# Optimization experiments

Measured on AMD Instinct MI355X. Metric: run time of the kernel, lower is better.

Reference implementation:

```python
import jax, jax.numpy as jnp
import numpy as np

# Junction tree: C0=(X0,X1f,X2), C1=(X1c,X2,X3f), C2=(X2,X3c,X4)
D0, D1F, D1C, D2, D3F, D3C, D4 = 256, 1024, 256, 256, 512, 256, 512


def _sel(fine: int, coarse: int) -> jnp.ndarray:
    """0/1 selection matrix [fine, coarse]: M[f, f // (fine//coarse)] = 1.
    Equivalent to torch_to_matrix_mul(arange(fine), arange(fine)//r, fine, coarse)."""
    r = fine // coarse
    return (jnp.arange(fine)[:, None] // r == jnp.arange(coarse)[None, :]).astype(jnp.float32)


def setup_inputs() -> dict:
    key = jax.random.key(0)
    k0, k1, k2 = jax.random.split(key, 3)
    theta0 = jax.random.normal(k0, (D0, D1F, D2), dtype=jnp.float32)
    theta1 = jax.random.normal(k1, (D1C, D2, D3F), dtype=jnp.float32)
    theta2 = jax.random.normal(k2, (D2, D3C, D4), dtype=jnp.float32)
    m_x1_fwd = _sel(D1F, D1C)          # (1024, 256): fine X1 -> coarse X1
    m_x1_bwd = m_x1_fwd.T              # (256, 1024): coarse X1 -> fine X1
    m_x3_fwd = _sel(D3F, D3C)          # (512, 256)
    m_x3_bwd = m_x3_fwd.T              # (256, 512)
    return dict(theta0=theta0, theta1=theta1, theta2=theta2,
                m_x1_fwd=m_x1_fwd, m_x1_bwd=m_x1_bwd,
                m_x3_fwd=m_x3_fwd, m_x3_bwd=m_x3_bwd)


def reference(theta0, theta1, theta2, m_x1_fwd, m_x1_bwd, m_x3_fwd, m_x3_bwd):
    # --- forward message C0 -> C1: sum over X0, map X1 fine->coarse, X2 passthrough
    msg01 = jnp.einsum('jc,jf->fc', theta0.sum(axis=0), m_x1_fwd)   # (D1C, D2)
    theta1 = theta1 + msg01[:, :, None]                             # reshape_dims (T,T,F)
    # --- forward message C1 -> C2: sum over X1, X2 passthrough, map X3 fine->coarse
    msg12 = jnp.einsum('cj,jf->cf', theta1.sum(axis=0), m_x3_fwd)   # (D2, D3C)
    theta2 = theta2 + msg12[:, :, None]
    # --- backward message C2 -> C1: sum over X4, subtract stored fwd msg, map X3 coarse->fine
    msg21 = jnp.einsum('cj,jf->cf', theta2.sum(axis=2) - msg12, m_x3_bwd)  # (D2, D3F)
    theta1 = theta1 + msg21[None, :, :]                             # reshape_dims (F,T,T)
    # --- backward message C1 -> C0: sum over X3, subtract stored fwd msg, map X1 coarse->fine
    msg10 = jnp.einsum('jc,jf->fc', theta1.sum(axis=2) - msg01, m_x1_bwd)  # (D1F, D2)
    theta0 = theta0 + msg10[None, :, :]
    return (theta0, theta1, theta2)
```

## Files before the change

### kernel.cpp

```cpp
#include <hip/hip_runtime.h>

#define D0   256
#define D1F  1024
#define D1C  256
#define D2   256
#define D3F  512
#define D3C  256
#define D4   512

#define OFF_MSG01 0
#define OFF_S10   65536
#define OFF_S12   196608
#define OFF_S22   262144
#define OFF_MSG12 327680
#define OFF_S2    393216
#define OFF_S3    458752

__global__ __launch_bounds__(256) void k_r0(const float* __restrict__ t0,
                                            float* __restrict__ ws) {
  float* msg01 = ws + OFF_MSG01;
  const int f = blockIdx.x, ic = blockIdx.y, t = threadIdx.x;
  const int c4 = t & 63, r = t >> 6;
  const float4* t0v = (const float4*)t0;
  const int j = 4 * f + r;
  float4 acc = make_float4(0.f, 0.f, 0.f, 0.f);
#pragma unroll
  for (int it = 0; it < 16; ++it) {
    const int i = ic * 16 + it;
    float4 v = t0v[((size_t)i * D1F + j) * 64 + c4];
    acc.x += v.x; acc.y += v.y; acc.z += v.z; acc.w += v.w;
  }
  __shared__ float4 lds[256];
  lds[t] = acc;
  __syncthreads();
  if (t < 64) {
    float4 a0 = lds[t], a1 = lds[t + 64], a2 = lds[t + 128], a3 = lds[t + 192];
    float* dst = &msg01[f * D2 + 4 * t];
    atomicAdd(dst + 0, a0.x + a1.x + a2.x + a3.x);
    atomicAdd(dst + 1, a0.y + a1.y + a2.y + a3.y);
    atomicAdd(dst + 2, a0.z + a1.z + a2.z + a3.z);
    atomicAdd(dst + 3, a0.w + a1.w + a2.w + a3.w);
  }
}

__global__ __launch_bounds__(256) void k_r1(const float* __restrict__ t1,
                                            float* __restrict__ ws) {
  float* S10 = ws + OFF_S10;
  float* S12 = ws + OFF_S12;
  const int c = blockIdx.x, ac = blockIdx.y, t = threadIdx.x;
  const int lane = t & 63, w = t >> 6;
  __shared__ float red[4];
  float sx = 0.f, sy = 0.f;
  for (int aa = 0; aa < 16; ++aa) {
    const int a = ac * 16 + aa;
    const float2* row = (const float2*)(t1 + ((size_t)a * D2 + c) * D3F);
    float2 v = row[t];
    sx += v.x; sy += v.y;
    float p = v.x + v.y;
#pragma unroll
    for (int off = 32; off; off >>= 1) p += __shfl_down(p, off);
    if (lane == 0) red[w] = p;
    __syncthreads();
    if (t == 0) S12[a * D2 + c] = red[0] + red[1] + red[2] + red[3];
    __syncthreads();
  }
  atomicAdd(&S10[c * D3F + 2 * t + 0], sx);
  atomicAdd(&S10[c * D3F + 2 * t + 1], sy);
}

__global__ __launch_bounds__(256) void k_msg12(float* __restrict__ ws) {
  const float* msg01 = ws + OFF_MSG01;
  const float* S10   = ws + OFF_S10;
  float* msg12       = ws + OFF_MSG12;
  const int c = blockIdx.x, t = threadIdx.x;
  float p = msg01[t * D2 + c];
#pragma unroll
  for (int off = 32; off; off >>= 1) p += __shfl_down(p, off);
  __shared__ float red[4];
  if ((t & 63) == 0) red[t >> 6] = p;
  __syncthreads();
  const float colA = red[0] + red[1] + red[2] + red[3];
  msg12[c * D3C + t] = S10[c * D3F + 2 * t] + S10[c * D3F + 2 * t + 1] + 2.f * colA;
}

__global__ __launch_bounds__(256) void k_w2(const float* __restrict__ t2,
                                            float* __restrict__ out2,
                                            float* __restrict__ ws) {
  const float* msg12 = ws + OFF_MSG12;
  float* S22         = ws + OFF_S22;
  const int c = blockIdx.x, fc = blockIdx.y, t = threadIdx.x;
  const int lane = t & 63, w = t >> 6;
  __shared__ float red[4];
  for (int ff = 0; ff < 16; ++ff) {
    const int f = fc * 16 + ff;
    const size_t base = ((size_t)c * D3C + f) * D4;
    float2 v = ((const float2*)(t2 + base))[t];
    const float m = msg12[c * D3C + f];
    float2 o; o.x = v.x + m; o.y = v.y + m;
    ((float2*)(out2 + base))[t] = o;
    float p = v.x + v.y;
#pragma unroll
    for (int off = 32; off; off >>= 1) p += __shfl_down(p, off);
    if (lane == 0) red[w] = p;
    __syncthreads();
    if (t == 0) S22[c * D3C + f] = red[0] + red[1] + red[2] + red[3];
    __syncthreads();
  }
}

__global__ __launch_bounds__(256) void k_s3(float* __restrict__ ws) {
  const float* msg01 = ws + OFF_MSG01;
  const float* S12   = ws + OFF_S12;
  const float* S22   = ws + OFF_S22;
  const float* msg12 = ws + OFF_MSG12;
  float* s2          = ws + OFF_S2;
  float* s3          = ws + OFF_S3;
  const int c = blockIdx.x, t = threadIdx.x;
  const float m12 = msg12[c * D3C + t];
  const float s2v = S22[c * D3C + t] + 511.f * m12;
  s2[c * D3C + t] = s2v;
  float p = s2v;
#pragma unroll
  for (int off = 32; off; off >>= 1) p += __shfl_down(p, off);
  __shared__ float red[4];
  if ((t & 63) == 0) red[t >> 6] = p;
  __syncthreads();
  const float rs = red[0] + red[1] + red[2] + red[3];
  s3[t * D2 + c] = S12[t * D2 + c] + 511.f * msg01[t * D2 + c] + 2.f * rs;
}

__global__ __launch_bounds__(256) void k_w1(const float* __restrict__ t1,
                                            float* __restrict__ out1,
                                            const float* __restrict__ ws) {
  const float* msg01 = ws + OFF_MSG01;
  const float* s2    = ws + OFF_S2;
  const size_t idx = (size_t)blockIdx.x * 256 + threadIdx.x;
  const int k4 = (int)(idx & 127);
  const int c  = (int)((idx >> 7) & 255);
  const int a  = (int)(idx >> 15);
  float4 v = ((const float4*)t1)[idx];
  const float m  = msg01[a * D2 + c];
  const float sa = s2[c * D3C + 2 * k4];
  const float sb = s2[c * D3C + 2 * k4 + 1];
  float4 o;
  o.x = v.x + m + sa; o.y = v.y + m + sa;
  o.z = v.z + m + sb; o.w = v.w + m + sb;
  ((float4*)out1)[idx] = o;
}

__global__ __launch_bounds__(256) void k_w0(const float* __restrict__ t0,
                                            float* __restrict__ out0,
                                            const float* __restrict__ ws) {
  const float4* s3v = (const float4*)(ws + OFF_S3);
  const size_t idx = (size_t)blockIdx.x * 256 + threadIdx.x;
  const int c4 = (int)(idx & 63);
  const int j  = (int)((idx >> 6) & 1023);
  float4 v = ((const float4*)t0)[idx];
  float4 m = s3v[(j >> 2) * 64 + c4];
  float4 o;
  o.x = v.x + m.x; o.y = v.y + m.y; o.z = v.z + m.z; o.w = v.w + m.w;
  ((float4*)out0)[idx] = o;
}

extern "C" void kernel_launch(void* const* d_in, const int* in_sizes, int n_in,
                              void* d_out, int out_size, void* d_ws, size_t ws_size,
                              hipStream_t stream) {
  const float* t0 = (const float*)d_in[0];
  const float* t1 = (const float*)d_in[1];
  const float* t2 = (const float*)d_in[2];
  float* out0 = (float*)d_out;
  float* out1 = out0 + (size_t)D0 * D1F * D2;
  float* out2 = out1 + (size_t)D1C * D2 * D3F;
  float* ws = (float*)d_ws;

  hipMemsetAsync(d_ws, 0, (size_t)OFF_S12 * sizeof(float), stream);

  k_r0<<<dim3(256, 16), 256, 0, stream>>>(t0, ws);
  k_r1<<<dim3(256, 16), 256, 0, stream>>>(t1, ws);
  k_msg12<<<256, 256, 0, stream>>>(ws);
  k_w2<<<dim3(256, 16), 256, 0, stream>>>(t2, out2, ws);
  k_s3<<<256, 256, 0, stream>>>(ws);
  k_w1<<<32768, 256, 0, stream>>>(t1, out1, ws);
  k_w0<<<65536, 256, 0, stream>>>(t0, out0, ws);
}
```

Measured before the change: 943.2 us.

## Chunk computation over X2 to reuse theta slices in cache and fuse kernels

Splits the whole pipeline into four chunks along the X2 axis so each chunk's theta0/theta1 slices are reduced and then rewritten while still likely resident in the large last-level cache. Merges the reduction kernels and message computations into fewer launches, and uses nontemporal stores for outputs to avoid polluting cache. Adds more launches and narrower per-row accesses in theta0 (64-byte segments), which may reduce coalescing efficiency.

Measured after the change: 958.0 us. Within noise of the previous version (+1.6%).

```diff
diff --git a/kernel.cpp b/kernel.cpp
--- a/kernel.cpp
+++ b/kernel.cpp
@@ -8,158 +8,180 @@
 #define D3C  256
 #define D4   512
 
+#define CB   64
+#define NCB  4
+
 #define OFF_MSG01 0
 #define OFF_S10   65536
 #define OFF_S12   196608
 #define OFF_S22   262144
 #define OFF_MSG12 327680
-#define OFF_S2    393216
-#define OFF_S3    458752
-
-__global__ __launch_bounds__(256) void k_r0(const float* __restrict__ t0,
-                                            float* __restrict__ ws) {
-  float* msg01 = ws + OFF_MSG01;
-  const int f = blockIdx.x, ic = blockIdx.y, t = threadIdx.x;
-  const int c4 = t & 63, r = t >> 6;
-  const float4* t0v = (const float4*)t0;
-  const int j = 4 * f + r;
-  float4 acc = make_float4(0.f, 0.f, 0.f, 0.f);
-#pragma unroll
-  for (int it = 0; it < 16; ++it) {
-    const int i = ic * 16 + it;
-    float4 v = t0v[((size_t)i * D1F + j) * 64 + c4];
-    acc.x += v.x; acc.y += v.y; acc.z += v.z; acc.w += v.w;
-  }
-  __shared__ float4 lds[256];
-  lds[t] = acc;
-  __syncthreads();
-  if (t < 64) {
-    float4 a0 = lds[t], a1 = lds[t + 64], a2 = lds[t + 128], a3 = lds[t + 192];
-    float* dst = &msg01[f * D2 + 4 * t];
-    atomicAdd(dst + 0, a0.x + a1.x + a2.x + a3.x);
-    atomicAdd(dst + 1, a0.y + a1.y + a2.y + a3.y);
-    atomicAdd(dst + 2, a0.z + a1.z + a2.z + a3.z);
-    atomicAdd(dst + 3, a0.w + a1.w + a2.w + a3.w);
-  }
-}
-
-__global__ __launch_bounds__(256) void k_r1(const float* __restrict__ t1,
-                                            float* __restrict__ ws) {
-  float* S10 = ws + OFF_S10;
-  float* S12 = ws + OFF_S12;
-  const int c = blockIdx.x, ac = blockIdx.y, t = threadIdx.x;
-  const int lane = t & 63, w = t >> 6;
+#define OFF_S3    393216
+
+typedef float f4 __attribute__((ext_vector_type(4)));
+
+__device__ __forceinline__ float wave_sum(float s) {
+#pragma unroll
+  for (int off = 32; off; off >>= 1) s += __shfl_down(s, off);
+  return s;
+}
+__device__ __forceinline__ float wave_allsum(float s) {
+#pragma unroll
+  for (int off = 32; off; off >>= 1) s += __shfl_xor(s, off);
+  return s;
+}
+
+__global__ __launch_bounds__(256) void k_stage1(const float* __restrict__ t0,
+                                                const float* __restrict__ t1,
+                                                float* __restrict__ ws, int cb) {
+  const int t = threadIdx.x, lane = t & 63, w = t >> 6;
+  __shared__ f4 lds[4][2][64];
+  if (blockIdx.x < 1024) {
+    const int bx = blockIdx.x;
+    const int c  = cb * CB + (bx & 63);
+    const int ac = bx >> 6;
+    float* S10 = ws + OFF_S10;
+    float* S12 = ws + OFF_S12;
+    f4 accA = {0.f, 0.f, 0.f, 0.f};
+    f4 accB = {0.f, 0.f, 0.f, 0.f};
+#pragma unroll
+    for (int ii = 0; ii < 4; ++ii) {
+      const int a = ac * 16 + ii * 4 + w;
+      const f4* row = (const f4*)(t1 + ((size_t)a * D2 + c) * D3F);
+      f4 v0 = row[lane];
+      f4 v1 = row[lane + 64];
+      accA += v0; accB += v1;
+      float s = v0.x + v0.y + v0.z + v0.w + v1.x + v1.y + v1.z + v1.w;
+      s = wave_sum(s);
+      if (lane == 0) S12[a * D2 + c] = s;
+    }
+    lds[w][0][lane] = accA;
+    lds[w][1][lane] = accB;
+    __syncthreads();
+    if (t < 128) {
+      const int which = t >> 6, l = t & 63;
+      f4 s = lds[0][which][l] + lds[1][which][l] + lds[2][which][l] + lds[3][which][l];
+      float* dst = &S10[(size_t)c * D3F + which * 256 + 4 * l];
+      atomicAdd(dst + 0, s.x);
+      atomicAdd(dst + 1, s.y);
+      atomicAdd(dst + 2, s.z);
+      atomicAdd(dst + 3, s.w);
+    }
+  } else {
+    const int bx = blockIdx.x - 1024;
+    const int f = bx & 255, ic = bx >> 8;
+    float* msg01 = ws + OFF_MSG01;
+    const int c4 = lane & 15, jr = lane >> 4;
+    const int j = 4 * f + jr;
+    const f4* t0v = (const f4*)t0;
+    f4 acc = {0.f, 0.f, 0.f, 0.f};
+#pragma unroll
+    for (int ii = 0; ii < 4; ++ii) {
+      const int i = ic * 16 + w * 4 + ii;
+      acc += t0v[((size_t)i * D1F + j) * 64 + cb * 16 + c4];
+    }
+#pragma unroll
+    for (int off = 32; off >= 16; off >>= 1) {
+      acc.x += __shfl_down(acc.x, off);
+      acc.y += __shfl_down(acc.y, off);
+      acc.z += __shfl_down(acc.z, off);
+      acc.w += __shfl_down(acc.w, off);
+    }
+    if (jr == 0) lds[w][0][c4] = acc;
+    __syncthreads();
+    if (t < 16) {
+      f4 s = lds[0][0][t] + lds[1][0][t] + lds[2][0][t] + lds[3][0][t];
+      float* dst = &msg01[f * D2 + cb * CB + 4 * t];
+      atomicAdd(dst + 0, s.x);
+      atomicAdd(dst + 1, s.y);
+      atomicAdd(dst + 2, s.z);
+      atomicAdd(dst + 3, s.w);
+    }
+  }
+}
+
+__global__ __launch_bounds__(256) void k_w2mm(const float* __restrict__ t2,
+                                              float* __restrict__ out2,
+                                              float* __restrict__ ws, int cb) {
+  const float* msg01 = ws + OFF_MSG01;
+  const float* S10   = ws + OFF_S10;
+  float* msg12 = ws + OFF_MSG12;
+  float* S22   = ws + OFF_S22;
+  const int bx = blockIdx.x;
+  const int c = cb * CB + (bx & 63), fc = bx >> 6;
+  const int t = threadIdx.x, lane = t & 63, w = t >> 6;
+  float p = msg01[lane * D2 + c] + msg01[(lane + 64) * D2 + c]
+          + msg01[(lane + 128) * D2 + c] + msg01[(lane + 192) * D2 + c];
+  p = wave_allsum(p);
+  const float* S10c = S10 + (size_t)c * D3F;
+#pragma unroll
+  for (int ii = 0; ii < 4; ++ii) {
+    const int f = fc * 16 + ii * 4 + w;
+    const float m = S10c[2 * f] + S10c[2 * f + 1] + 2.f * p;
+    if (lane == 0) msg12[c * D3C + f] = m;
+    const size_t base4 = ((size_t)c * D3C + f) * (D4 / 4);
+    const f4* row = (const f4*)t2 + base4;
+    f4* orow = (f4*)out2 + base4;
+    f4 v0 = __builtin_nontemporal_load(row + lane);
+    f4 v1 = __builtin_nontemporal_load(row + lane + 64);
+    __builtin_nontemporal_store(v0 + m, orow + lane);
+    __builtin_nontemporal_store(v1 + m, orow + lane + 64);
+    float s = v0.x + v0.y + v0.z + v0.w + v1.x + v1.y + v1.z + v1.w;
+    s = wave_sum(s);
+    if (lane == 0) S22[c * D3C + f] = s;
+  }
+}
+
+__global__ __launch_bounds__(256) void k_w1s3(const float* __restrict__ t1,
+                                              float* __restrict__ out1,
+                                              float* __restrict__ ws, int cb) {
+  const float* msg01 = ws + OFF_MSG01;
+  const float* S22   = ws + OFF_S22;
+  const float* msg12 = ws + OFF_MSG12;
+  const int t = threadIdx.x;
   __shared__ float red[4];
-  float sx = 0.f, sy = 0.f;
-  for (int aa = 0; aa < 16; ++aa) {
-    const int a = ac * 16 + aa;
-    const float2* row = (const float2*)(t1 + ((size_t)a * D2 + c) * D3F);
-    float2 v = row[t];
-    sx += v.x; sy += v.y;
-    float p = v.x + v.y;
-#pragma unroll
-    for (int off = 32; off; off >>= 1) p += __shfl_down(p, off);
+  if (blockIdx.x < 8192) {
+    const size_t idx = (size_t)blockIdx.x * 256 + t;
+    const int k4 = (int)(idx & 127);
+    const int cl = (int)((idx >> 7) & 63);
+    const int a  = (int)(idx >> 13);
+    const int c  = cb * CB + cl;
+    const size_t addr = ((size_t)a * D2 + c) * (D3F / 4) + k4;
+    f4 v = ((const f4*)t1)[addr];
+    const float m = msg01[a * D2 + c];
+    const float2 s22v = ((const float2*)S22)[c * 128 + k4];
+    const float2 m12v = ((const float2*)msg12)[c * 128 + k4];
+    const float s2a = m + s22v.x + 511.f * m12v.x;
+    const float s2b = m + s22v.y + 511.f * m12v.y;
+    f4 o;
+    o.x = v.x + s2a; o.y = v.y + s2a; o.z = v.z + s2b; o.w = v.w + s2b;
+    __builtin_nontemporal_store(o, (f4*)out1 + addr);
+  } else {
+    const float* S12 = ws + OFF_S12;
+    float* s3 = ws + OFF_S3;
+    const int c = cb * CB + (int)(blockIdx.x - 8192);
+    const int lane = t & 63, w = t >> 6;
+    const float s2v = S22[c * D3C + t] + 511.f * msg12[c * D3C + t];
+    float p = wave_sum(s2v);
     if (lane == 0) red[w] = p;
     __syncthreads();
-    if (t == 0) S12[a * D2 + c] = red[0] + red[1] + red[2] + red[3];
-    __syncthreads();
-  }
-  atomicAdd(&S10[c * D3F + 2 * t + 0], sx);
-  atomicAdd(&S10[c * D3F + 2 * t + 1], sy);
-}
-
-__global__ __launch_bounds__(256) void k_msg12(float* __restrict__ ws) {
-  const float* msg01 = ws + OFF_MSG01;
-  const float* S10   = ws + OFF_S10;
-  float* msg12       = ws + OFF_MSG12;
-  const int c = blockIdx.x, t = threadIdx.x;
-  float p = msg01[t * D2 + c];
-#pragma unroll
-  for (int off = 32; off; off >>= 1) p += __shfl_down(p, off);
-  __shared__ float red[4];
-  if ((t & 63) == 0) red[t >> 6] = p;
-  __syncthreads();
-  const float colA = red[0] + red[1] + red[2] + red[3];
-  msg12[c * D3C + t] = S10[c * D3F + 2 * t] + S10[c * D3F + 2 * t + 1] + 2.f * colA;
-}
-
-__global__ __launch_bounds__(256) void k_w2(const float* __restrict__ t2,
-                                            float* __restrict__ out2,
-                                            float* __restrict__ ws) {
-  const float* msg12 = ws + OFF_MSG12;
-  float* S22         = ws + OFF_S22;
-  const int c = blockIdx.x, fc = blockIdx.y, t = threadIdx.x;
-  const int lane = t & 63, w = t >> 6;
-  __shared__ float red[4];
-  for (int ff = 0; ff < 16; ++ff) {
-    const int f = fc * 16 + ff;
-    const size_t base = ((size_t)c * D3C + f) * D4;
-    float2 v = ((const float2*)(t2 + base))[t];
-    const float m = msg12[c * D3C + f];
-    float2 o; o.x = v.x + m; o.y = v.y + m;
-    ((float2*)(out2 + base))[t] = o;
-    float p = v.x + v.y;
-#pragma unroll
-    for (int off = 32; off; off >>= 1) p += __shfl_down(p, off);
-    if (lane == 0) red[w] = p;
-    __syncthreads();
-    if (t == 0) S22[c * D3C + f] = red[0] + red[1] + red[2] + red[3];
-    __syncthreads();
-  }
-}
-
-__global__ __launch_bounds__(256) void k_s3(float* __restrict__ ws) {
-  const float* msg01 = ws + OFF_MSG01;
-  const float* S12   = ws + OFF_S12;
-  const float* S22   = ws + OFF_S22;
-  const float* msg12 = ws + OFF_MSG12;
-  float* s2          = ws + OFF_S2;
-  float* s3          = ws + OFF_S3;
-  const int c = blockIdx.x, t = threadIdx.x;
-  const float m12 = msg12[c * D3C + t];
-  const float s2v = S22[c * D3C + t] + 511.f * m12;
-  s2[c * D3C + t] = s2v;
-  float p = s2v;
-#pragma unroll
-  for (int off = 32; off; off >>= 1) p += __shfl_down(p, off);
-  __shared__ float red[4];
-  if ((t & 63) == 0) red[t >> 6] = p;
-  __syncthreads();
-  const float rs = red[0] + red[1] + red[2] + red[3];
-  s3[t * D2 + c] = S12[t * D2 + c] + 511.f * msg01[t * D2 + c] + 2.f * rs;
-}
-
-__global__ __launch_bounds__(256) void k_w1(const float* __restrict__ t1,
-                                            float* __restrict__ out1,
-                                            const float* __restrict__ ws) {
-  const float* msg01 = ws + OFF_MSG01;
-  const float* s2    = ws + OFF_S2;
-  const size_t idx = (size_t)blockIdx.x * 256 + threadIdx.x;
-  const int k4 = (int)(idx & 127);
-  const int c  = (int)((idx >> 7) & 255);
-  const int a  = (int)(idx >> 15);
-  float4 v = ((const float4*)t1)[idx];
-  const float m  = msg01[a * D2 + c];
-  const float sa = s2[c * D3C + 2 * k4];
-  const float sb = s2[c * D3C + 2 * k4 + 1];
-  float4 o;
-  o.x = v.x + m + sa; o.y = v.y + m + sa;
-  o.z = v.z + m + sb; o.w = v.w + m + sb;
-  ((float4*)out1)[idx] = o;
+    const float rs = red[0] + red[1] + red[2] + red[3];
+    s3[t * D2 + c] = S12[t * D2 + c] + 511.f * msg01[t * D2 + c] + 2.f * rs;
+  }
 }
 
 __global__ __launch_bounds__(256) void k_w0(const float* __restrict__ t0,
                                             float* __restrict__ out0,
-                                            const float* __restrict__ ws) {
-  const float4* s3v = (const float4*)(ws + OFF_S3);
+                                            const float* __restrict__ ws, int cb) {
+  const f4* s3v = (const f4*)(ws + OFF_S3);
   const size_t idx = (size_t)blockIdx.x * 256 + threadIdx.x;
-  const int c4 = (int)(idx & 63);
-  const int j  = (int)((idx >> 6) & 1023);
-  float4 v = ((const float4*)t0)[idx];
-  float4 m = s3v[(j >> 2) * 64 + c4];
-  float4 o;
-  o.x = v.x + m.x; o.y = v.y + m.y; o.z = v.z + m.z; o.w = v.w + m.w;
-  ((float4*)out0)[idx] = o;
+  const int c4 = (int)(idx & 15);
+  const int j  = (int)((idx >> 4) & 1023);
+  const int i  = (int)(idx >> 14);
+  const size_t addr = ((size_t)i * D1F + j) * 64 + cb * 16 + c4;
+  f4 v = ((const f4*)t0)[addr];
+  f4 m = s3v[(j >> 2) * 64 + cb * 16 + c4];
+  __builtin_nontemporal_store(v + m, (f4*)out0 + addr);
 }
 
 extern "C" void kernel_launch(void* const* d_in, const int* in_sizes, int n_in,
@@ -175,11 +197,10 @@
 
   hipMemsetAsync(d_ws, 0, (size_t)OFF_S12 * sizeof(float), stream);
 
-  k_r0<<<dim3(256, 16), 256, 0, stream>>>(t0, ws);
-  k_r1<<<dim3(256, 16), 256, 0, stream>>>(t1, ws);
-  k_msg12<<<256, 256, 0, stream>>>(ws);
-  k_w2<<<dim3(256, 16), 256, 0, stream>>>(t2, out2, ws);
-  k_s3<<<256, 256, 0, stream>>>(ws);
-  k_w1<<<32768, 256, 0, stream>>>(t1, out1, ws);
-  k_w0<<<65536, 256, 0, stream>>>(t0, out0, ws);
-}
+  for (int cb = 0; cb < NCB; ++cb) {
+    k_stage1<<<5120, 256, 0, stream>>>(t0, t1, ws, cb);
+    k_w2mm<<<1024, 256, 0, stream>>>(t2, out2, ws, cb);
+    k_w1s3<<<8256, 256, 0, stream>>>(t1, out1, ws, cb);
+    k_w0<<<16384, 256, 0, stream>>>(t0, out0, ws, cb);
+  }
+}
```
